# Kernel optimization log

Hardware: AMD Instinct MI355X
Metric: run time of the kernel (lower is better)

## Reference

```python
import jax, jax.numpy as jnp
import numpy as np

N_NODES = 50000
N_EDGES = 500000
D = 128  # in_size == out_size


def setup_inputs() -> dict:
    key = jax.random.key(0)
    ks = jax.random.split(key, 12)
    s = 1.0 / np.sqrt(D)
    feats = jax.random.normal(ks[0], (N_NODES, D), dtype=jnp.float32)
    # per-etype Linear params (torch Linear: y = x @ W.T + b)
    W_chem = jax.random.uniform(ks[1], (D, D), jnp.float32, -s, s)
    b_chem = jax.random.uniform(ks[2], (D,), jnp.float32, -s, s)
    W_elec = jax.random.uniform(ks[3], (D, D), jnp.float32, -s, s)
    b_elec = jax.random.uniform(ks[4], (D,), jnp.float32, -s, s)
    W_out = jax.random.uniform(ks[5], (D, D), jnp.float32, -s, s)
    b_out = jax.random.uniform(ks[6], (D,), jnp.float32, -s, s)
    src_chem = jax.random.randint(ks[7], (N_EDGES,), 0, N_NODES, dtype=jnp.int32)
    dst_chem = jax.random.randint(ks[8], (N_EDGES,), 0, N_NODES, dtype=jnp.int32)
    src_elec = jax.random.randint(ks[9], (N_EDGES,), 0, N_NODES, dtype=jnp.int32)
    dst_elec = jax.random.randint(ks[10], (N_EDGES,), 0, N_NODES, dtype=jnp.int32)
    return {
        "feats": feats,
        "W_chem": W_chem, "b_chem": b_chem,
        "W_elec": W_elec, "b_elec": b_elec,
        "W_out": W_out, "b_out": b_out,
        "src_chem": src_chem, "dst_chem": dst_chem,
        "src_elec": src_elec, "dst_elec": dst_elec,
    }


def reference(feats, W_chem, b_chem, W_elec, b_elec, W_out, b_out,
              src_chem, dst_chem, src_elec, dst_elec):
    n = feats.shape[0]
    # Per-etype linear projection of all node features
    Wh_chem = feats @ W_chem.T + b_chem  # [N, D]
    Wh_elec = feats @ W_elec.T + b_elec  # [N, D]
    # copy_src + sum scatter-aggregation per etype, merged with 'sum'
    h = jax.ops.segment_sum(Wh_chem[src_chem], dst_chem, num_segments=n)
    h = h + jax.ops.segment_sum(Wh_elec[src_elec], dst_elec, num_segments=n)
    # output Linear plus the last-iterated etype's Wh (quirk of original code:
    # 'electrical' is last in etypes order)
    return h @ W_out.T + b_out + Wh_elec
```

## Files before the change

### kernel.cpp

```cpp
#include <hip/hip_runtime.h>

#define D 128
#define PAD 48

typedef __attribute__((ext_vector_type(8))) short bf16x8;
typedef __attribute__((ext_vector_type(4))) float f32x4;

__device__ __forceinline__ unsigned short f2bf(float x) {
    unsigned int u = __float_as_uint(x);
    u += 0x7fffu + ((u >> 16) & 1u);
    return (unsigned short)(u >> 16);
}
__device__ __forceinline__ unsigned int pk2(float lo, float hi) {
    return ((unsigned int)f2bf(hi) << 16) | (unsigned int)f2bf(lo);
}
__device__ __forceinline__ float bf_lo(unsigned int u) { return __uint_as_float(u << 16); }
__device__ __forceinline__ float bf_hi(unsigned int u) { return __uint_as_float(u & 0xffff0000u); }

#define ACC8(U, P, Q)                                   \
        P.x += bf_lo(U.x); P.y += bf_hi(U.x);           \
        P.z += bf_lo(U.y); P.w += bf_hi(U.y);           \
        Q.x += bf_lo(U.z); Q.y += bf_hi(U.z);           \
        Q.z += bf_lo(U.w); Q.w += bf_hi(U.w);

__global__ __launch_bounds__(256) void wzero(
    const float* __restrict__ Wc, const float* __restrict__ We,
    const float* __restrict__ Wo, const float* __restrict__ b_c,
    const float* __restrict__ b_e, const float* __restrict__ b_o,
    unsigned short* __restrict__ wall, float* __restrict__ bco,
    float* __restrict__ beo, float* __restrict__ bsum,
    int* __restrict__ cnt, int nzero) {
    const int id = blockIdx.x * 256 + threadIdx.x;
    for (int i = id; i < nzero; i += gridDim.x * 256) cnt[i] = 0;
    if (id < 16384) {
        const int j = id >> 7, k = id & 127;
        float s1 = 0.f, s2 = 0.f;
        for (int m = 0; m < 128; ++m) {
            float wo = Wo[j * 128 + m];
            s1 = fmaf(wo, Wc[m * 128 + k], s1);
            s2 = fmaf(wo, We[m * 128 + k], s2);
        }
        wall[j * 128 + k]         = f2bf(s1);
        wall[16384 + j * 128 + k] = f2bf(s2);
        wall[32768 + j * 128 + k] = f2bf(We[j * 128 + k]);
        if (k == 0) {
            float t1 = 0.f, t2 = 0.f;
            for (int m = 0; m < 128; ++m) {
                float wo = Wo[j * 128 + m];
                t1 = fmaf(wo, b_c[m], t1);
                t2 = fmaf(wo, b_e[m], t2);
            }
            bco[j] = t1; beo[j] = t2; bsum[j] = b_o[j] + b_e[j];
        }
    }
}

__global__ __launch_bounds__(256) void fillp(
    const float4* __restrict__ f, uint4* __restrict__ o, int n8,
    const int* __restrict__ sc, const int* __restrict__ dc,
    const int* __restrict__ se, const int* __restrict__ de,
    int* __restrict__ cnt, unsigned short* __restrict__ csr, int E, int N) {
    int i = blockIdx.x * 256 + threadIdx.x;
    if (i < n8) {
        float4 a = f[2 * i];
        float4 b = f[2 * i + 1];
        o[i] = make_uint4(pk2(a.x, a.y), pk2(a.z, a.w), pk2(b.x, b.y), pk2(b.z, b.w));
    }
    if (i < 2 * E) {
        int d, s;
        if (i < E) { d = dc[i];         s = sc[i]; }
        else       { d = de[i - E] + N; s = se[i - E]; }
        int pos = atomicAdd(&cnt[d], 1);
        if (pos < PAD) csr[(size_t)d * PAD + pos] = (unsigned short)s;
    }
}

__global__ __launch_bounds__(1024) void aggregate_bf(const unsigned short* __restrict__ fbf,
                                                     const unsigned short* __restrict__ csr,
                                                     const int* __restrict__ cnt,
                                                     unsigned short* __restrict__ S, int N2) {
    const int wv  = threadIdx.x >> 6;
    const int ln  = threadIdx.x & 63;
    const int sub = ln >> 4;
    const int l16 = ln & 15;
    const int v   = blockIdx.x * 64 + wv * 4 + sub;
    if (v < N2) {
        const int deg = min(cnt[v], PAD);
        const unsigned short* row = csr + (size_t)v * PAD;
        const int off = l16 * 8;
        float4 a0 = make_float4(0.f,0.f,0.f,0.f), b0 = make_float4(0.f,0.f,0.f,0.f);
        float4 a1 = make_float4(0.f,0.f,0.f,0.f), b1 = make_float4(0.f,0.f,0.f,0.f);
        float4 a2 = make_float4(0.f,0.f,0.f,0.f), b2 = make_float4(0.f,0.f,0.f,0.f);
        float4 a3 = make_float4(0.f,0.f,0.f,0.f), b3 = make_float4(0.f,0.f,0.f,0.f);
        int e = 0;
        for (; e + 4 <= deg; e += 4) {
            int i0 = row[e + 0];
            int i1 = row[e + 1];
            int i2 = row[e + 2];
            int i3 = row[e + 3];
            uint4 u0 = *(const uint4*)(fbf + (size_t)i0 * D + off);
            uint4 u1 = *(const uint4*)(fbf + (size_t)i1 * D + off);
            uint4 u2 = *(const uint4*)(fbf + (size_t)i2 * D + off);
            uint4 u3 = *(const uint4*)(fbf + (size_t)i3 * D + off);
            ACC8(u0, a0, b0) ACC8(u1, a1, b1) ACC8(u2, a2, b2) ACC8(u3, a3, b3)
        }
        for (; e < deg; ++e) {
            int sv = row[e];
            uint4 u = *(const uint4*)(fbf + (size_t)sv * D + off);
            ACC8(u, a0, b0)
        }
        a0.x += a1.x + a2.x + a3.x;  a0.y += a1.y + a2.y + a3.y;
        a0.z += a1.z + a2.z + a3.z;  a0.w += a1.w + a2.w + a3.w;
        b0.x += b1.x + b2.x + b3.x;  b0.y += b1.y + b2.y + b3.y;
        b0.z += b1.z + b2.z + b3.z;  b0.w += b1.w + b2.w + b3.w;
        uint4 o;
        o.x = pk2(a0.x, a0.y); o.y = pk2(a0.z, a0.w);
        o.z = pk2(b0.x, b0.y); o.w = pk2(b0.z, b0.w);
        *(uint4*)(S + (size_t)v * D + off) = o;
    }
}

__global__ __launch_bounds__(256, 4) void gemm_bg(
    const unsigned short* __restrict__ S,
    const unsigned short* __restrict__ fbf,
    const unsigned short* __restrict__ wall,
    const float* __restrict__ bco, const float* __restrict__ beo,
    const float* __restrict__ bsum,
    const int* __restrict__ degc, const int* __restrict__ dege,
    float* __restrict__ out, int M) {
    __shared__ unsigned int At[64 * 64];

    const int t    = threadIdx.x;
    const int r0   = blockIdx.x * 64;
    const int w    = t >> 6;
    const int lane = t & 63;
    const int ln   = lane & 15;
    const int quad = lane >> 4;
    const int lnx  = ln & 7;

    const int rowA = (w * 16 + ln) * 64;
    const unsigned short* wB = wall + (size_t)ln * 128 + quad * 8;

    f32x4 acc[8];
#pragma unroll
    for (int g = 0; g < 8; ++g) acc[g] = (f32x4){0.f, 0.f, 0.f, 0.f};

#define STAGE(ASRC)                                                             \
    {                                                                           \
        _Pragma("unroll") for (int i2 = 0; i2 < 4; ++i2) {                      \
            int g2 = i2 * 256 + t;                                              \
            int m  = g2 >> 4;                                                   \
            int cc = g2 & 15;                                                   \
            int r  = r0 + m;                                                    \
            uint4 v = make_uint4(0u, 0u, 0u, 0u);                               \
            if (r < M) v = *(const uint4*)((ASRC) + (size_t)r * 128 + cc * 8);  \
            *(uint4*)(At + m * 64 + ((cc ^ (m & 7)) << 2)) = v;                 \
        }                                                                       \
    }

#define KSTEP(P, KS)                                                                 \
    {                                                                                \
        const int cx = ((((KS) * 4 + quad) ^ lnx) << 2);                             \
        bf16x8 a = *(const bf16x8*)(At + rowA + cx);                                 \
        _Pragma("unroll") for (int g = 0; g < 8; ++g) {                              \
            bf16x8 b = *(const bf16x8*)(wB + (P) * 16384 + g * 2048 + (KS) * 32);    \
            acc[g] = __builtin_amdgcn_mfma_f32_16x16x32_bf16(a, b, acc[g], 0, 0, 0); \
        }                                                                            \
    }

    STAGE(S)
    __syncthreads();
    KSTEP(0, 0) KSTEP(0, 1) KSTEP(0, 2) KSTEP(0, 3)
    __syncthreads();
    STAGE(S + (size_t)M * 128)
    __syncthreads();
    KSTEP(1, 0) KSTEP(1, 1) KSTEP(1, 2) KSTEP(1, 3)
    __syncthreads();
    STAGE(fbf)
    __syncthreads();
    KSTEP(2, 0) KSTEP(2, 1) KSTEP(2, 2) KSTEP(2, 3)

    float dcv[4], dev[4];
    int   rrv[4];
#pragma unroll
    for (int rg = 0; rg < 4; ++rg) {
        const int rr = r0 + w * 16 + quad * 4 + rg;
        rrv[rg] = rr;
        dcv[rg] = (rr < M) ? (float)degc[rr] : 0.f;
        dev[rg] = (rr < M) ? (float)dege[rr] : 0.f;
    }
#pragma unroll
    for (int g = 0; g < 8; ++g) {
        const int col = g * 16 + ln;
        const float bc = bco[col], be = beo[col], bs = bsum[col];
#pragma unroll
        for (int rg = 0; rg < 4; ++rg) {
            if (rrv[rg] < M) {
                out[(size_t)rrv[rg] * 128 + col] =
                    acc[g][rg] + bs + dcv[rg] * bc + dev[rg] * be;
            }
        }
    }
#undef KSTEP
#undef STAGE
}


extern "C" void kernel_launch(void* const* d_in, const int* in_sizes, int n_in,
                              void* d_out, int out_size, void* d_ws, size_t ws_size,
                              hipStream_t stream) {
    const float* feats  = (const float*)d_in[0];
    const float* W_chem = (const float*)d_in[1];
    const float* b_chem = (const float*)d_in[2];
    const float* W_elec = (const float*)d_in[3];
    const float* b_elec = (const float*)d_in[4];
    const float* W_out  = (const float*)d_in[5];
    const float* b_out  = (const float*)d_in[6];
    const int* src_chem = (const int*)d_in[7];
    const int* dst_chem = (const int*)d_in[8];
    const int* src_elec = (const int*)d_in[9];
    const int* dst_elec = (const int*)d_in[10];
    float* out = (float*)d_out;

    const int N = in_sizes[0] / D;
    const int E = in_sizes[7];
    const int N2 = 2 * N;

    unsigned short* fbf  = (unsigned short*)d_ws;
    unsigned short* S    = fbf + (size_t)N * D;
    unsigned short* wall = S + (size_t)N2 * D;
    float* bco  = (float*)(wall + 3 * 16384);
    float* beo  = bco + 128;
    float* bsum = beo + 128;
    int* cnt    = (int*)(bsum + 128);
    unsigned short* csr = (unsigned short*)(cnt + N2);

    const int n8 = N * D / 8;

    wzero<<<512, 256, 0, stream>>>(W_chem, W_elec, W_out, b_chem, b_elec, b_out,
                                   wall, bco, beo, bsum, cnt, N2);
    fillp<<<(2 * E + 255) / 256, 256, 0, stream>>>(
        (const float4*)feats, (uint4*)fbf, n8,
        src_chem, dst_chem, src_elec, dst_elec, cnt, csr, E, N);
    aggregate_bf<<<(N2 + 63) / 64, 1024, 0, stream>>>(fbf, csr, cnt, S, N2);
    gemm_bg<<<(N + 63) / 64, 256, 0, stream>>>(S, fbf, wall, bco, beo, bsum,
                                               cnt, cnt + N, out, N);
}
```

Before: 258.0 us.

## Overlap electrical-edge CSR fill with chemical-edge aggregation in one kernel

The edge bucketing is split by edge type. The first kernel converts features to bf16 and fills only the chemical CSR. A new combined kernel interleaves blocks that scatter electrical edges into their CSR with blocks that aggregate the already-complete chemical rows, and a final aggregate pass handles the electrical rows. The aim is to hide the latency-bound atomic scatter behind the gather-bound aggregation instead of running them in separate phases. The cost is one extra kernel launch and a more complex block-index mapping.

```diff
diff --git a/kernel.cpp b/kernel.cpp
--- a/kernel.cpp
+++ b/kernel.cpp
@@ -22,6 +22,44 @@
         P.z += bf_lo(U.y); P.w += bf_hi(U.y);           \
         Q.x += bf_lo(U.z); Q.y += bf_hi(U.z);           \
         Q.z += bf_lo(U.w); Q.w += bf_hi(U.w);
+
+__device__ __forceinline__ void agg_row(const unsigned short* __restrict__ fbf,
+                                        const unsigned short* __restrict__ csr,
+                                        const int* __restrict__ cnt,
+                                        unsigned short* __restrict__ S,
+                                        int v, int off) {
+    const int deg = min(cnt[v], PAD);
+    const unsigned short* row = csr + (size_t)v * PAD;
+    float4 a0 = make_float4(0.f,0.f,0.f,0.f), b0 = make_float4(0.f,0.f,0.f,0.f);
+    float4 a1 = make_float4(0.f,0.f,0.f,0.f), b1 = make_float4(0.f,0.f,0.f,0.f);
+    float4 a2 = make_float4(0.f,0.f,0.f,0.f), b2 = make_float4(0.f,0.f,0.f,0.f);
+    float4 a3 = make_float4(0.f,0.f,0.f,0.f), b3 = make_float4(0.f,0.f,0.f,0.f);
+    int e = 0;
+    for (; e + 4 <= deg; e += 4) {
+        int i0 = row[e + 0];
+        int i1 = row[e + 1];
+        int i2 = row[e + 2];
+        int i3 = row[e + 3];
+        uint4 u0 = *(const uint4*)(fbf + (size_t)i0 * D + off);
+        uint4 u1 = *(const uint4*)(fbf + (size_t)i1 * D + off);
+        uint4 u2 = *(const uint4*)(fbf + (size_t)i2 * D + off);
+        uint4 u3 = *(const uint4*)(fbf + (size_t)i3 * D + off);
+        ACC8(u0, a0, b0) ACC8(u1, a1, b1) ACC8(u2, a2, b2) ACC8(u3, a3, b3)
+    }
+    for (; e < deg; ++e) {
+        int sv = row[e];
+        uint4 u = *(const uint4*)(fbf + (size_t)sv * D + off);
+        ACC8(u, a0, b0)
+    }
+    a0.x += a1.x + a2.x + a3.x;  a0.y += a1.y + a2.y + a3.y;
+    a0.z += a1.z + a2.z + a3.z;  a0.w += a1.w + a2.w + a3.w;
+    b0.x += b1.x + b2.x + b3.x;  b0.y += b1.y + b2.y + b3.y;
+    b0.z += b1.z + b2.z + b3.z;  b0.w += b1.w + b2.w + b3.w;
+    uint4 o;
+    o.x = pk2(a0.x, a0.y); o.y = pk2(a0.z, a0.w);
+    o.z = pk2(b0.x, b0.y); o.w = pk2(b0.z, b0.w);
+    *(uint4*)(S + (size_t)v * D + off) = o;
+}
 
 __global__ __launch_bounds__(256) void wzero(
     const float* __restrict__ Wc, const float* __restrict__ We,
@@ -55,69 +93,61 @@
     }
 }
 
-__global__ __launch_bounds__(256) void fillp(
+__global__ __launch_bounds__(256) void fillcv(
     const float4* __restrict__ f, uint4* __restrict__ o, int n8,
     const int* __restrict__ sc, const int* __restrict__ dc,
-    const int* __restrict__ se, const int* __restrict__ de,
-    int* __restrict__ cnt, unsigned short* __restrict__ csr, int E, int N) {
+    int* __restrict__ cnt, unsigned short* __restrict__ csr, int E) {
     int i = blockIdx.x * 256 + threadIdx.x;
     if (i < n8) {
         float4 a = f[2 * i];
         float4 b = f[2 * i + 1];
         o[i] = make_uint4(pk2(a.x, a.y), pk2(a.z, a.w), pk2(b.x, b.y), pk2(b.z, b.w));
     }
-    if (i < 2 * E) {
-        int d, s;
-        if (i < E) { d = dc[i];         s = sc[i]; }
-        else       { d = de[i - E] + N; s = se[i - E]; }
+    if (i < E) {
+        int d = dc[i], s = sc[i];
         int pos = atomicAdd(&cnt[d], 1);
         if (pos < PAD) csr[(size_t)d * PAD + pos] = (unsigned short)s;
+    }
+}
+
+__global__ __launch_bounds__(256) void fe_ac(
+    const unsigned short* __restrict__ fbf,
+    const int* __restrict__ se, const int* __restrict__ de,
+    int* __restrict__ cnt, unsigned short* __restrict__ csr,
+    unsigned short* __restrict__ S,
+    int E, int N, int nf, int total) {
+    const int bid = blockIdx.x;
+    const int f0 = (int)(((long long)bid * nf) / total);
+    const int f1 = (int)(((long long)(bid + 1) * nf) / total);
+    if (f1 > f0) {
+        const int i = f0 * 256 + threadIdx.x;
+        if (i < E) {
+            int d = de[i] + N, s = se[i];
+            int pos = atomicAdd(&cnt[d], 1);
+            if (pos < PAD) csr[(size_t)d * PAD + pos] = (unsigned short)s;
+        }
+    } else {
+        const int aidx = bid - f0;
+        const int wv  = threadIdx.x >> 6;
+        const int ln  = threadIdx.x & 63;
+        const int sub = ln >> 4;
+        const int l16 = ln & 15;
+        const int v = aidx * 16 + wv * 4 + sub;
+        if (v < N) agg_row(fbf, csr, cnt, S, v, l16 * 8);
     }
 }
 
 __global__ __launch_bounds__(1024) void aggregate_bf(const unsigned short* __restrict__ fbf,
                                                      const unsigned short* __restrict__ csr,
                                                      const int* __restrict__ cnt,
-                                                     unsigned short* __restrict__ S, int N2) {
+                                                     unsigned short* __restrict__ S,
+                                                     int base, int nend) {
     const int wv  = threadIdx.x >> 6;
     const int ln  = threadIdx.x & 63;
     const int sub = ln >> 4;
     const int l16 = ln & 15;
-    const int v   = blockIdx.x * 64 + wv * 4 + sub;
-    if (v < N2) {
-        const int deg = min(cnt[v], PAD);
-        const unsigned short* row = csr + (size_t)v * PAD;
-        const int off = l16 * 8;
-        float4 a0 = make_float4(0.f,0.f,0.f,0.f), b0 = make_float4(0.f,0.f,0.f,0.f);
-        float4 a1 = make_float4(0.f,0.f,0.f,0.f), b1 = make_float4(0.f,0.f,0.f,0.f);
-        float4 a2 = make_float4(0.f,0.f,0.f,0.f), b2 = make_float4(0.f,0.f,0.f,0.f);
-        float4 a3 = make_float4(0.f,0.f,0.f,0.f), b3 = make_float4(0.f,0.f,0.f,0.f);
-        int e = 0;
-        for (; e + 4 <= deg; e += 4) {
-            int i0 = row[e + 0];
-            int i1 = row[e + 1];
-            int i2 = row[e + 2];
-            int i3 = row[e + 3];
-            uint4 u0 = *(const uint4*)(fbf + (size_t)i0 * D + off);
-            uint4 u1 = *(const uint4*)(fbf + (size_t)i1 * D + off);
-            uint4 u2 = *(const uint4*)(fbf + (size_t)i2 * D + off);
-            uint4 u3 = *(const uint4*)(fbf + (size_t)i3 * D + off);
-            ACC8(u0, a0, b0) ACC8(u1, a1, b1) ACC8(u2, a2, b2) ACC8(u3, a3, b3)
-        }
-        for (; e < deg; ++e) {
-            int sv = row[e];
-            uint4 u = *(const uint4*)(fbf + (size_t)sv * D + off);
-            ACC8(u, a0, b0)
-        }
-        a0.x += a1.x + a2.x + a3.x;  a0.y += a1.y + a2.y + a3.y;
-        a0.z += a1.z + a2.z + a3.z;  a0.w += a1.w + a2.w + a3.w;
-        b0.x += b1.x + b2.x + b3.x;  b0.y += b1.y + b2.y + b3.y;
-        b0.z += b1.z + b2.z + b3.z;  b0.w += b1.w + b2.w + b3.w;
-        uint4 o;
-        o.x = pk2(a0.x, a0.y); o.y = pk2(a0.z, a0.w);
-        o.z = pk2(b0.x, b0.y); o.w = pk2(b0.z, b0.w);
-        *(uint4*)(S + (size_t)v * D + off) = o;
-    }
+    const int v   = base + blockIdx.x * 64 + wv * 4 + sub;
+    if (v < nend) agg_row(fbf, csr, cnt, S, v, l16 * 8);
 }
 
 __global__ __launch_bounds__(256, 4) void gemm_bg(
@@ -236,13 +266,17 @@
     unsigned short* csr = (unsigned short*)(cnt + N2);
 
     const int n8 = N * D / 8;
+    const int nf = (E + 255) / 256;
+    const int na = (N + 15) / 16;
+    const int total = nf + na;
 
     wzero<<<512, 256, 0, stream>>>(W_chem, W_elec, W_out, b_chem, b_elec, b_out,
                                    wall, bco, beo, bsum, cnt, N2);
-    fillp<<<(2 * E + 255) / 256, 256, 0, stream>>>(
-        (const float4*)feats, (uint4*)fbf, n8,
-        src_chem, dst_chem, src_elec, dst_elec, cnt, csr, E, N);
-    aggregate_bf<<<(N2 + 63) / 64, 1024, 0, stream>>>(fbf, csr, cnt, S, N2);
+    fillcv<<<(n8 + 255) / 256, 256, 0, stream>>>(
+        (const float4*)feats, (uint4*)fbf, n8, src_chem, dst_chem, cnt, csr, E);
+    fe_ac<<<total, 256, 0, stream>>>(fbf, src_elec, dst_elec, cnt, csr, S,
+                                     E, N, nf, total);
+    aggregate_bf<<<(N + 63) / 64, 1024, 0, stream>>>(fbf, csr, cnt, S, N, N2);
     gemm_bg<<<(N + 63) / 64, 256, 0, stream>>>(S, fbf, wall, bco, beo, bsum,
                                                cnt, cnt + N, out, N);
 }
```

New measurement: 251.1 us. 2.7% less time.
